# Performance work log

Measured on AMD Instinct MI355X. Metric: run time of the kernel, lower is better.

The kernel has to match this reference:

```python
import jax, jax.numpy as jnp
import numpy as np

EMBED_K = 64
DISEN_K = [4, 4]           # channels per layer
WEIGHT_SIZE_LIST = [64, 64, 64]
TEMPERATURE = 1.0
ROUTING_ITERATIONS = 3
N_LAYERS = 2
EPS = 1e-12


def setup_inputs() -> dict:
    key = jax.random.key(0)
    ks = jax.random.split(key, 8)
    num_users, num_items = 500000, 200000
    n_neigh = 4096
    params = {}
    for layer in range(N_LAYERS):
        k_ch = DISEN_K[layer]
        d_in = WEIGHT_SIZE_LIST[layer]
        d_out = WEIGHT_SIZE_LIST[layer + 1] // k_ch
        params[f"W{layer}"] = jax.random.normal(ks[4 + layer], (k_ch, d_in, d_out), dtype=jnp.float32) * 0.1
        params[f"b{layer}"] = jnp.zeros((k_ch, d_out), dtype=jnp.float32)
    return {
        "user": 123,
        "item": 77,
        "neigh_user": jax.random.randint(ks[0], (n_neigh,), 0, num_items),   # item ids
        "neigh_item": jax.random.randint(ks[1], (n_neigh,), 0, num_users),   # user ids
        "Gu": jax.random.normal(ks[2], (num_users, EMBED_K), dtype=jnp.float32) * 0.1,
        "Gi": jax.random.normal(ks[3], (num_items, EMBED_K), dtype=jnp.float32) * 0.1,
        **params,
    }


def _project(x, W, b):
    # FeatureProjection: per-channel linear + relu. x: [N, d_in] -> [N, K, d_out]
    return jax.nn.relu(jnp.einsum('ni,kid->nkd', x, W) + b)


def _route_once(z):
    # One DisenGCNLayer call on star graph: node 0 = ego, nodes 1..N = neighbors.
    # L2-normalize per channel (torch F.normalize p=2, dim=-1)
    nrm = jnp.maximum(jnp.linalg.norm(z, axis=-1, keepdims=True), EPS)
    zn = z / nrm                              # [N+1, K, d]
    ego = zn[0]                               # [K, d]
    nb = zn[1:]                               # [N, K, d]
    # routing probs: softmax over channels K of similarity / temperature
    p = jax.nn.softmax(jnp.einsum('nkd,kd->nk', nb, ego) / TEMPERATURE, axis=-1)
    # aggregated ego capsule per channel
    return jnp.einsum('nk,nkd->kd', p, nb)    # [K, d]


def _forward(Gu, Gi, W0, b0, W1, b1, user, item, neigh_user, neigh_item):
    # ego user + its item neighbors; ego item + its user neighbors
    eu = jnp.concatenate([Gu[user][None, :], Gi[neigh_user]], axis=0)   # [N+1, 64]
    ei = jnp.concatenate([Gi[item][None, :], Gu[neigh_item]], axis=0)   # [N+1, 64]
    for (W, b) in ((W0, b0), (W1, b1)):
        zu = _project(eu, W, b)               # [N+1, K, d]
        zi = _project(ei, W, b)
        for _ in range(ROUTING_ITERATIONS):
            zu = zu.at[0].set(_route_once(zu))
            zi = zi.at[0].set(_route_once(zi))
        eu = zu.reshape(zu.shape[0], -1)      # [N+1, K*d]
        ei = zi.reshape(zi.shape[0], -1)
        # message dropout = 0.0 -> identity
    xui = jnp.sum(eu[0] * ei[0])[None]        # shape (1,)
    return xui, eu[0], ei[0]


def reference(user, item, neigh_user, neigh_item, Gu, Gi, W0, b0, W1, b1):
    return _forward(Gu, Gi, W0, b0, W1, b1, user, item, neigh_user, neigh_item)
```

## Files before the change

### kernel.cpp

```cpp
#include <hip/hip_runtime.h>
#include <hip/hip_bf16.h>


#define EPS 1e-12f
#define LOG2E 1.44269504088896f
#define SPB 8
#define NBK (2 * SPB)

__device__ __forceinline__ float g16sum(float v) {
    v += __shfl_xor(v, 1, 64);
    v += __shfl_xor(v, 2, 64);
    v += __shfl_xor(v, 4, 64);
    v += __shfl_xor(v, 8, 64);
    return v;
}
__device__ __forceinline__ unsigned short f2bf(float f) {
    unsigned int b = __float_as_uint(f);
    b += 0x7fffu + ((b >> 16) & 1u);
    return (unsigned short)(b >> 16);
}
__device__ __forceinline__ float bf2f(unsigned short u) {
    return __uint_as_float(((unsigned int)u) << 16);
}
__device__ __forceinline__ float bflo(unsigned int w) {
    return __uint_as_float(w << 16);
}
__device__ __forceinline__ float bfhi(unsigned int w) {
    return __uint_as_float(w & 0xffff0000u);
}

__device__ __forceinline__ void slot_write(unsigned long long* p, float v,
                                           unsigned int gen) {
    atomicExch(p, ((unsigned long long)__float_as_uint(v) << 32) |
                  (unsigned long long)gen);
}
__device__ __forceinline__ float slot_read(unsigned long long* p,
                                           unsigned int gen) {
    unsigned long long v;
    for (;;) {
        v = atomicAdd(p, 0ull);
        if ((unsigned int)(v & 0xffffffffull) == gen) break;
        __builtin_amdgcn_s_sleep(1);
    }
    return __uint_as_float((unsigned int)(v >> 32));
}

__device__ __forceinline__ float proj_row4(const float xa[4],
                                           const float* __restrict__ W,
                                           const float* __restrict__ b, int lane) {
    const int k = lane >> 4, d = lane & 15;
    float sum = b[k * 16 + d];
    const float* __restrict__ Wp = W + k * 1024 + d;
#pragma unroll
    for (int i = 0; i < 64; ++i)
        sum = fmaf(__shfl(xa[i & 3], i >> 2, 64), Wp[i * 16], sum);
    return fmaxf(sum, 0.f);
}

__global__ __launch_bounds__(256) void k1_gather_proj2(
    const int* __restrict__ user, const int* __restrict__ item,
    const int* __restrict__ nu, const int* __restrict__ ni,
    const float* __restrict__ Gu, const float* __restrict__ Gi,
    const float* __restrict__ W0, const float* __restrict__ b0,
    const float* __restrict__ W1, const float* __restrict__ b1,
    unsigned short* __restrict__ znbA, unsigned short* __restrict__ znbB,
    unsigned int* __restrict__ call_ctr, int n_rows)
{
    if (blockIdx.x == 0 && threadIdx.x == 0) atomicAdd(call_ctr, 1u);

    const int lane = threadIdx.x & 63;
    const int wv   = threadIdx.x >> 6;
    const int rr   = blockIdx.x * 4 + wv;
    if (rr >= 2 * n_rows) return;
    const int side = rr >= n_rows;
    const int n    = rr - side * n_rows;
    const int c    = lane & 15;

    int idx; const float* G;
    if (n == 0) { idx = side ? item[0] : user[0];     G = side ? Gi : Gu; }
    else        { idx = side ? ni[n - 1] : nu[n - 1]; G = side ? Gu : Gi; }
    const float4 xv = ((const float4*)(G + (size_t)idx * 64))[c];
    const float xa[4] = {xv.x, xv.y, xv.z, xv.w};

    const float z0 = proj_row4(xa, W0, b0, lane);
    const float nrm0 = fmaxf(sqrtf(g16sum(z0 * z0)), EPS);
    znbA[(size_t)rr * 64 + lane] = f2bf(z0 / nrm0);

    if (n == 0) return;

    float xa2[4];
#pragma unroll
    for (int jj = 0; jj < 4; ++jj) xa2[jj] = __shfl(z0, (c << 2) | jj, 64);
    const float z1 = proj_row4(xa2, W1, b1, lane);
    const float nrm1 = fmaxf(sqrtf(g16sum(z1 * z1)), EPS);
    znbB[(size_t)rr * 64 + lane] = f2bf(z1 / nrm1);
}

__global__ __launch_bounds__(1024) void k2_route_all(
    const unsigned short* __restrict__ znbA, const unsigned short* __restrict__ znbB,
    const float* __restrict__ W1, const float* __restrict__ b1,
    unsigned long long* __restrict__ slots,
    const unsigned int* __restrict__ call_ctr,
    float* __restrict__ out, int n_neigh)
{
    const int n_rows = n_neigh + 1;
    const int tid  = threadIdx.x;
    const int lane = tid & 63;
    const int wv   = tid >> 6;
    const int side = blockIdx.x & 1;
    const int bg   = blockIdx.x >> 1;
    const unsigned short* __restrict__ zA = znbA + (size_t)side * n_rows * 64;
    const unsigned short* __restrict__ zB = znbB + (size_t)side * n_rows * 64;
    const unsigned int genbase = (*call_ctr) * 8u;

    __shared__ float sW[4096];
    __shared__ float red[16][64];
    __shared__ float sEgo[64];
    __shared__ float sTmp[64];

    for (int q = tid; q < 4096; q += 1024) {
        const int i = q >> 6, m = q & 63;
        sW[q] = W1[(m >> 4) * 1024 + i * 16 + (m & 15)];
    }
    if (tid < 64) sEgo[tid] = bf2f(zA[tid]) * LOG2E;
    __syncthreads();

    const int j   = lane & 7;
    const int rg0 = bg * 128 + (tid >> 3);

    for (int s = 0; s < 6; ++s) {
        const unsigned short* __restrict__ zb = (s < 3) ? zA : zB;
        const unsigned int gen = genbase + (unsigned int)s + 1u;
        float ego[8];
#pragma unroll
        for (int m = 0; m < 8; ++m) ego[m] = sEgo[j * 8 + m];

        float a8[8] = {0.f, 0.f, 0.f, 0.f, 0.f, 0.f, 0.f, 0.f};
        for (int r = rg0; r < n_neigh; r += SPB * 128) {
            const uint4 q = *(const uint4*)(zb + (((size_t)r + 1) << 6) + (j << 3));
            float x[8];
            x[0] = bflo(q.x); x[1] = bfhi(q.x);
            x[2] = bflo(q.y); x[3] = bfhi(q.y);
            x[4] = bflo(q.z); x[5] = bfhi(q.z);
            x[6] = bflo(q.w); x[7] = bfhi(q.w);
            float partial = 0.f;
#pragma unroll
            for (int m = 0; m < 8; ++m) partial = fmaf(x[m], ego[m], partial);
            const float dp = partial + __shfl_xor(partial, 1, 64);
            const float eo = exp2f(dp);
            float den = eo + __shfl_xor(eo, 2, 64);
            den += __shfl_xor(den, 4, 64);
            const float p = eo * __builtin_amdgcn_rcpf(den);
#pragma unroll
            for (int m = 0; m < 8; ++m) a8[m] = fmaf(p, x[m], a8[m]);
        }
#pragma unroll
        for (int mask = 8; mask <= 32; mask <<= 1)
#pragma unroll
            for (int m = 0; m < 8; ++m) a8[m] += __shfl_xor(a8[m], mask, 64);
        if (lane < 8) {
#pragma unroll
            for (int m = 0; m < 8; ++m) red[wv][lane * 8 + m] = a8[m];
        }
        __syncthreads();

        unsigned long long* slotbase = slots + (size_t)(s * 2 + side) * SPB * 64;
        if (wv == 0) {
            float ssum = 0.f;
#pragma unroll
            for (int w = 0; w < 16; ++w) ssum += red[w][lane];
            slot_write(&slotbase[bg * 64 + lane], ssum, gen);
        }
        __syncthreads();

        if (s < 5) {
            if (wv < SPB)
                red[wv][lane] = slot_read(&slotbase[wv * 64 + lane], gen);
            __syncthreads();
            if (wv == 0) {
                float e = 0.f;
#pragma unroll
                for (int bb = 0; bb < SPB; ++bb) e += red[bb][lane];
                if (s == 2) sTmp[lane] = e;
                else sEgo[lane] = (e / fmaxf(sqrtf(g16sum(e * e)), EPS)) * LOG2E;
            }
            __syncthreads();
            if (s == 2) {
                if (wv == 0) {
                    float xa[4];
#pragma unroll
                    for (int jj = 0; jj < 4; ++jj) xa[jj] = sTmp[((lane & 15) << 2) | jj];
                    float sum = b1[lane];
#pragma unroll
                    for (int i = 0; i < 64; ++i)
                        sum = fmaf(__shfl(xa[i & 3], i >> 2, 64), sW[i * 64 + lane], sum);
                    sum = fmaxf(sum, 0.f);
                    sEgo[lane] = (sum / fmaxf(sqrtf(g16sum(sum * sum)), EPS)) * LOG2E;
                }
                __syncthreads();
            }
        } else if (side == 0 && bg == 0) {
            const int s2 = wv >> 3, bb = wv & 7;
            unsigned long long* sb2 = slots + (size_t)(5 * 2 + s2) * SPB * 64;
            red[wv][lane] = slot_read(&sb2[bb * 64 + lane], gen);
            __syncthreads();
            if (wv == 0) {
                float u = 0.f, v = 0.f;
#pragma unroll
                for (int w = 0; w < 8; ++w)  u += red[w][lane];
#pragma unroll
                for (int w = 8; w < 16; ++w) v += red[w][lane];
                out[1 + lane]  = u;
                out[65 + lane] = v;
                float p = u * v;
#pragma unroll
                for (int sh = 32; sh >= 1; sh >>= 1) p += __shfl_xor(p, sh, 64);
                if (lane == 0) out[0] = p;
            }
        }
    }
}

extern "C" void kernel_launch(void* const* d_in, const int* in_sizes, int n_in,
                              void* d_out, int out_size, void* d_ws, size_t ws_size,
                              hipStream_t stream) {
    const int*   user       = (const int*)d_in[0];
    const int*   item       = (const int*)d_in[1];
    const int*   neigh_user = (const int*)d_in[2];
    const int*   neigh_item = (const int*)d_in[3];
    const float* Gu         = (const float*)d_in[4];
    const float* Gi         = (const float*)d_in[5];
    const float* W0         = (const float*)d_in[6];
    const float* b0         = (const float*)d_in[7];
    const float* W1         = (const float*)d_in[8];
    const float* b1         = (const float*)d_in[9];
    float* out = (float*)d_out;

    const int n_neigh = in_sizes[2];
    const int n_rows  = n_neigh + 1;
    const size_t rowsz = (size_t)2 * n_rows * 64;

    unsigned short*     znbA  = (unsigned short*)d_ws;
    unsigned short*     znbB  = znbA + rowsz;
    unsigned long long* slots = (unsigned long long*)(znbB + rowsz);
    unsigned int*       ctr   = (unsigned int*)(slots + 6 * 2 * SPB * 64);

    hipLaunchKernelGGL(k1_gather_proj2, dim3((2 * n_rows + 3) / 4), dim3(256), 0, stream,
                       user, item, neigh_user, neigh_item, Gu, Gi, W0, b0, W1, b1,
                       znbA, znbB, ctr, n_rows);
    hipLaunchKernelGGL(k2_route_all, dim3(NBK), dim3(1024), 0, stream,
                       znbA, znbB, W1, b1, slots, ctr, out, n_neigh);
}
```

Measured before the change: 45.46 us.

## Fuse gather, projections and routing into one kernel with LDS-resident neighbor rows

Merges the gather/projection kernel into the routing kernel so each of the 16 blocks gathers its own 512 neighbor rows, projects them with W0 from shared memory, and keeps the bf16 results in LDS with a padded stride. Per-row normalization for layer 0 is moved into the routing loop, and the layer-1 projection is done in place in LDS after the third routing step. This removes a kernel launch and the global round-trip of the intermediate buffers. The cost is that only 16 blocks now do all the gather and projection work, so parallelism for the memory-bound gather drops sharply. The per-call generation counters also become per block.

```diff
diff --git a/kernel.cpp b/kernel.cpp
--- a/kernel.cpp
+++ b/kernel.cpp
@@ -6,6 +6,7 @@
 #define LOG2E 1.44269504088896f
 #define SPB 8
 #define NBK (2 * SPB)
+#define ZSTR 80
 
 __device__ __forceinline__ float g16sum(float v) {
     v += __shfl_xor(v, 1, 64);
@@ -28,7 +29,6 @@
 __device__ __forceinline__ float bfhi(unsigned int w) {
     return __uint_as_float(w & 0xffff0000u);
 }
-
 __device__ __forceinline__ void slot_write(unsigned long long* p, float v,
                                            unsigned int gen) {
     atomicExch(p, ((unsigned long long)__float_as_uint(v) << 32) |
@@ -45,114 +45,128 @@
     return __uint_as_float((unsigned int)(v >> 32));
 }
 
-__device__ __forceinline__ float proj_row4(const float xa[4],
-                                           const float* __restrict__ W,
-                                           const float* __restrict__ b, int lane) {
-    const int k = lane >> 4, d = lane & 15;
-    float sum = b[k * 16 + d];
-    const float* __restrict__ Wp = W + k * 1024 + d;
-#pragma unroll
-    for (int i = 0; i < 64; ++i)
-        sum = fmaf(__shfl(xa[i & 3], i >> 2, 64), Wp[i * 16], sum);
-    return fmaxf(sum, 0.f);
-}
-
-__global__ __launch_bounds__(256) void k1_gather_proj2(
+__global__ __launch_bounds__(1024, 1) void disen_one(
     const int* __restrict__ user, const int* __restrict__ item,
     const int* __restrict__ nu, const int* __restrict__ ni,
     const float* __restrict__ Gu, const float* __restrict__ Gi,
     const float* __restrict__ W0, const float* __restrict__ b0,
     const float* __restrict__ W1, const float* __restrict__ b1,
-    unsigned short* __restrict__ znbA, unsigned short* __restrict__ znbB,
-    unsigned int* __restrict__ call_ctr, int n_rows)
-{
-    if (blockIdx.x == 0 && threadIdx.x == 0) atomicAdd(call_ctr, 1u);
-
-    const int lane = threadIdx.x & 63;
-    const int wv   = threadIdx.x >> 6;
-    const int rr   = blockIdx.x * 4 + wv;
-    if (rr >= 2 * n_rows) return;
-    const int side = rr >= n_rows;
-    const int n    = rr - side * n_rows;
-    const int c    = lane & 15;
-
-    int idx; const float* G;
-    if (n == 0) { idx = side ? item[0] : user[0];     G = side ? Gi : Gu; }
-    else        { idx = side ? ni[n - 1] : nu[n - 1]; G = side ? Gu : Gi; }
-    const float4 xv = ((const float4*)(G + (size_t)idx * 64))[c];
-    const float xa[4] = {xv.x, xv.y, xv.z, xv.w};
-
-    const float z0 = proj_row4(xa, W0, b0, lane);
-    const float nrm0 = fmaxf(sqrtf(g16sum(z0 * z0)), EPS);
-    znbA[(size_t)rr * 64 + lane] = f2bf(z0 / nrm0);
-
-    if (n == 0) return;
-
-    float xa2[4];
-#pragma unroll
-    for (int jj = 0; jj < 4; ++jj) xa2[jj] = __shfl(z0, (c << 2) | jj, 64);
-    const float z1 = proj_row4(xa2, W1, b1, lane);
-    const float nrm1 = fmaxf(sqrtf(g16sum(z1 * z1)), EPS);
-    znbB[(size_t)rr * 64 + lane] = f2bf(z1 / nrm1);
-}
-
-__global__ __launch_bounds__(1024) void k2_route_all(
-    const unsigned short* __restrict__ znbA, const unsigned short* __restrict__ znbB,
-    const float* __restrict__ W1, const float* __restrict__ b1,
-    unsigned long long* __restrict__ slots,
-    const unsigned int* __restrict__ call_ctr,
+    unsigned long long* __restrict__ slots, unsigned int* __restrict__ ctr,
     float* __restrict__ out, int n_neigh)
 {
-    const int n_rows = n_neigh + 1;
     const int tid  = threadIdx.x;
     const int lane = tid & 63;
     const int wv   = tid >> 6;
     const int side = blockIdx.x & 1;
     const int bg   = blockIdx.x >> 1;
-    const unsigned short* __restrict__ zA = znbA + (size_t)side * n_rows * 64;
-    const unsigned short* __restrict__ zB = znbB + (size_t)side * n_rows * 64;
-    const unsigned int genbase = (*call_ctr) * 8u;
+    const int g    = lane >> 4;
+    const int c    = lane & 15;
+    const int j    = lane & 7;
 
     __shared__ float sW[4096];
     __shared__ float red[16][64];
     __shared__ float sEgo[64];
     __shared__ float sTmp[64];
-
+    __shared__ unsigned int sGen;
+    __shared__ unsigned short zB[512 * ZSTR];
+
+    if (tid == 0) sGen = (atomicAdd(&ctr[blockIdx.x], 1u) + 1u) * 8u;
+
+    for (int q = tid; q < 4096; q += 1024) {
+        const int i = q >> 6, m = q & 63;
+        sW[q] = W0[(m >> 4) * 1024 + i * 16 + (m & 15)];
+    }
+    __syncthreads();
+    const unsigned int genbase = sGen;
+
+    const int*   nidx = side ? ni : nu;
+    const float* G    = side ? Gu : Gi;
+    float4 xv[8];
+#pragma unroll
+    for (int pass = 0; pass < 8; ++pass) {
+        const int L = pass * 64 + wv * 4 + g;
+        const int n = 1 + bg * 128 + (L & 127) + (L >> 7) * (SPB * 128);
+        if (n <= n_neigh)
+            xv[pass] = ((const float4*)(G + (size_t)nidx[n - 1] * 64))[c];
+        else
+            xv[pass] = make_float4(0.f, 0.f, 0.f, 0.f);
+    }
+    {
+        const float4 bv = ((const float4*)b0)[c];
+#pragma unroll
+        for (int pass = 0; pass < 8; ++pass) {
+            const int L = pass * 64 + wv * 4 + g;
+            const bool act = (1 + bg * 128 + (L & 127) + (L >> 7) * (SPB * 128)) <= n_neigh;
+            float xa[4] = {xv[pass].x, xv[pass].y, xv[pass].z, xv[pass].w};
+            float o0 = bv.x, o1 = bv.y, o2 = bv.z, o3 = bv.w;
+#pragma unroll
+            for (int i = 0; i < 64; ++i) {
+                const float xi = __shfl(xa[i & 3], (g << 4) + (i >> 2), 64);
+                const float4 w = ((const float4*)sW)[i * 16 + c];
+                o0 = fmaf(xi, w.x, o0); o1 = fmaf(xi, w.y, o1);
+                o2 = fmaf(xi, w.z, o2); o3 = fmaf(xi, w.w, o3);
+            }
+            ushort4 st;
+            if (act) {
+                st.x = f2bf(fmaxf(o0, 0.f)); st.y = f2bf(fmaxf(o1, 0.f));
+                st.z = f2bf(fmaxf(o2, 0.f)); st.w = f2bf(fmaxf(o3, 0.f));
+            } else st = make_ushort4(0, 0, 0, 0);
+            *(ushort4*)&zB[L * ZSTR + 4 * c] = st;
+        }
+    }
+    if (wv == 0) {
+        const int idx0 = side ? item[0] : user[0];
+        const float* G0 = side ? Gi : Gu;
+        const float4 q0 = ((const float4*)(G0 + (size_t)idx0 * 64))[c];
+        float xa[4] = {q0.x, q0.y, q0.z, q0.w};
+        float s = b0[lane];
+#pragma unroll
+        for (int i = 0; i < 64; ++i)
+            s = fmaf(__shfl(xa[i & 3], i >> 2, 64), sW[i * 64 + lane], s);
+        s = fmaxf(s, 0.f);
+        sEgo[lane] = (s / fmaxf(sqrtf(g16sum(s * s)), EPS)) * LOG2E;
+    }
+    __syncthreads();
     for (int q = tid; q < 4096; q += 1024) {
         const int i = q >> 6, m = q & 63;
         sW[q] = W1[(m >> 4) * 1024 + i * 16 + (m & 15)];
     }
-    if (tid < 64) sEgo[tid] = bf2f(zA[tid]) * LOG2E;
     __syncthreads();
 
-    const int j   = lane & 7;
-    const int rg0 = bg * 128 + (tid >> 3);
-
     for (int s = 0; s < 6; ++s) {
-        const unsigned short* __restrict__ zb = (s < 3) ? zA : zB;
         const unsigned int gen = genbase + (unsigned int)s + 1u;
         float ego[8];
 #pragma unroll
         for (int m = 0; m < 8; ++m) ego[m] = sEgo[j * 8 + m];
 
         float a8[8] = {0.f, 0.f, 0.f, 0.f, 0.f, 0.f, 0.f, 0.f};
-        for (int r = rg0; r < n_neigh; r += SPB * 128) {
-            const uint4 q = *(const uint4*)(zb + (((size_t)r + 1) << 6) + (j << 3));
+#pragma unroll
+        for (int m = 0; m < 4; ++m) {
+            const int L = m * 128 + (tid >> 3);
+            const uint4 q = *(const uint4*)&zB[L * ZSTR + 8 * j];
             float x[8];
             x[0] = bflo(q.x); x[1] = bfhi(q.x);
             x[2] = bflo(q.y); x[3] = bfhi(q.y);
             x[4] = bflo(q.z); x[5] = bfhi(q.z);
             x[6] = bflo(q.w); x[7] = bfhi(q.w);
+            float inv = 1.f;
+            if (s < 3) {
+                float ss = 0.f;
+#pragma unroll
+                for (int mm = 0; mm < 8; ++mm) ss = fmaf(x[mm], x[mm], ss);
+                ss += __shfl_xor(ss, 1, 64);
+                inv = __builtin_amdgcn_rcpf(fmaxf(sqrtf(ss), EPS));
+            }
             float partial = 0.f;
 #pragma unroll
-            for (int m = 0; m < 8; ++m) partial = fmaf(x[m], ego[m], partial);
-            const float dp = partial + __shfl_xor(partial, 1, 64);
+            for (int mm = 0; mm < 8; ++mm) partial = fmaf(x[mm], ego[mm], partial);
+            const float dp = (partial + __shfl_xor(partial, 1, 64)) * inv;
             const float eo = exp2f(dp);
             float den = eo + __shfl_xor(eo, 2, 64);
             den += __shfl_xor(den, 4, 64);
-            const float p = eo * __builtin_amdgcn_rcpf(den);
-#pragma unroll
-            for (int m = 0; m < 8; ++m) a8[m] = fmaf(p, x[m], a8[m]);
+            const float p = eo * __builtin_amdgcn_rcpf(den) * inv;
+#pragma unroll
+            for (int mm = 0; mm < 8; ++mm) a8[mm] = fmaf(p, x[mm], a8[mm]);
         }
 #pragma unroll
         for (int mask = 8; mask <= 32; mask <<= 1)
@@ -172,6 +186,37 @@
             slot_write(&slotbase[bg * 64 + lane], ssum, gen);
         }
         __syncthreads();
+
+        if (s == 2) {
+            const float4 bv1 = ((const float4*)b1)[c];
+#pragma unroll
+            for (int pass = 0; pass < 8; ++pass) {
+                const int L = pass * 64 + wv * 4 + g;
+                const bool act = (1 + bg * 128 + (L & 127) + (L >> 7) * (SPB * 128)) <= n_neigh;
+                const ushort4 u = *(const ushort4*)&zB[L * ZSTR + 4 * c];
+                float xa[4] = {bf2f(u.x), bf2f(u.y), bf2f(u.z), bf2f(u.w)};
+                float o0 = bv1.x, o1 = bv1.y, o2 = bv1.z, o3 = bv1.w;
+#pragma unroll
+                for (int i = 0; i < 64; ++i) {
+                    const float xi = __shfl(xa[i & 3], (g << 4) + (i >> 2), 64);
+                    const float4 w = ((const float4*)sW)[i * 16 + c];
+                    o0 = fmaf(xi, w.x, o0); o1 = fmaf(xi, w.y, o1);
+                    o2 = fmaf(xi, w.z, o2); o3 = fmaf(xi, w.w, o3);
+                }
+                o0 = fmaxf(o0, 0.f); o1 = fmaxf(o1, 0.f);
+                o2 = fmaxf(o2, 0.f); o3 = fmaxf(o3, 0.f);
+                float ss = o0 * o0 + o1 * o1 + o2 * o2 + o3 * o3;
+                ss += __shfl_xor(ss, 1, 64);
+                ss += __shfl_xor(ss, 2, 64);
+                const float inv = __builtin_amdgcn_rcpf(fmaxf(sqrtf(ss), EPS));
+                ushort4 st;
+                if (act) {
+                    st.x = f2bf(o0 * inv); st.y = f2bf(o1 * inv);
+                    st.z = f2bf(o2 * inv); st.w = f2bf(o3 * inv);
+                } else st = make_ushort4(0, 0, 0, 0);
+                *(ushort4*)&zB[L * ZSTR + 4 * c] = st;
+            }
+        }
 
         if (s < 5) {
             if (wv < SPB)
@@ -199,7 +244,7 @@
                 }
                 __syncthreads();
             }
-        } else if (side == 0 && bg == 0) {
+        } else if (blockIdx.x == 0) {
             const int s2 = wv >> 3, bb = wv & 7;
             unsigned long long* sb2 = slots + (size_t)(5 * 2 + s2) * SPB * 64;
             red[wv][lane] = slot_read(&sb2[bb * 64 + lane], gen);
@@ -237,17 +282,11 @@
     float* out = (float*)d_out;
 
     const int n_neigh = in_sizes[2];
-    const int n_rows  = n_neigh + 1;
-    const size_t rowsz = (size_t)2 * n_rows * 64;
-
-    unsigned short*     znbA  = (unsigned short*)d_ws;
-    unsigned short*     znbB  = znbA + rowsz;
-    unsigned long long* slots = (unsigned long long*)(znbB + rowsz);
+
+    unsigned long long* slots = (unsigned long long*)d_ws;
     unsigned int*       ctr   = (unsigned int*)(slots + 6 * 2 * SPB * 64);
 
-    hipLaunchKernelGGL(k1_gather_proj2, dim3((2 * n_rows + 3) / 4), dim3(256), 0, stream,
-                       user, item, neigh_user, neigh_item, Gu, Gi, W0, b0, W1, b1,
-                       znbA, znbB, ctr, n_rows);
-    hipLaunchKernelGGL(k2_route_all, dim3(NBK), dim3(1024), 0, stream,
-                       znbA, znbB, W1, b1, slots, ctr, out, n_neigh);
-}
+    hipLaunchKernelGGL(disen_one, dim3(NBK), dim3(1024), 0, stream,
+                       user, item, neigh_user, neigh_item, Gu, Gi,
+                       W0, b0, W1, b1, slots, ctr, out, n_neigh);
+}
```

After: 123.1 us. 2.71x slower.

## Process four rows per wavefront with float4 weight loads in projection kernel

Applied to the files above, without the earlier changes.

The gather-and-project kernel now assigns four rows to each wavefront. Each 16-lane group owns one row and each lane computes four output features using float4 weight loads, where before each wave handled one row with one output per lane. This cuts the weight-load instructions per row and the number of blocks launched by four, and uses ushort4 stores. The trade-off is more registers per lane. The ego-row branch now runs the second projection redundantly, with its store masked off.

```diff
diff --git a/kernel.cpp b/kernel.cpp
--- a/kernel.cpp
+++ b/kernel.cpp
@@ -43,18 +43,6 @@
         __builtin_amdgcn_s_sleep(1);
     }
     return __uint_as_float((unsigned int)(v >> 32));
-}
-
-__device__ __forceinline__ float proj_row4(const float xa[4],
-                                           const float* __restrict__ W,
-                                           const float* __restrict__ b, int lane) {
-    const int k = lane >> 4, d = lane & 15;
-    float sum = b[k * 16 + d];
-    const float* __restrict__ Wp = W + k * 1024 + d;
-#pragma unroll
-    for (int i = 0; i < 64; ++i)
-        sum = fmaf(__shfl(xa[i & 3], i >> 2, 64), Wp[i * 16], sum);
-    return fmaxf(sum, 0.f);
 }
 
 __global__ __launch_bounds__(256) void k1_gather_proj2(
@@ -70,30 +58,78 @@
 
     const int lane = threadIdx.x & 63;
     const int wv   = threadIdx.x >> 6;
-    const int rr   = blockIdx.x * 4 + wv;
-    if (rr >= 2 * n_rows) return;
-    const int side = rr >= n_rows;
-    const int n    = rr - side * n_rows;
+    const int g    = lane >> 4;
     const int c    = lane & 15;
-
-    int idx; const float* G;
-    if (n == 0) { idx = side ? item[0] : user[0];     G = side ? Gi : Gu; }
-    else        { idx = side ? ni[n - 1] : nu[n - 1]; G = side ? Gu : Gi; }
-    const float4 xv = ((const float4*)(G + (size_t)idx * 64))[c];
-    const float xa[4] = {xv.x, xv.y, xv.z, xv.w};
-
-    const float z0 = proj_row4(xa, W0, b0, lane);
-    const float nrm0 = fmaxf(sqrtf(g16sum(z0 * z0)), EPS);
-    znbA[(size_t)rr * 64 + lane] = f2bf(z0 / nrm0);
-
-    if (n == 0) return;
-
-    float xa2[4];
-#pragma unroll
-    for (int jj = 0; jj < 4; ++jj) xa2[jj] = __shfl(z0, (c << 2) | jj, 64);
-    const float z1 = proj_row4(xa2, W1, b1, lane);
-    const float nrm1 = fmaxf(sqrtf(g16sum(z1 * z1)), EPS);
-    znbB[(size_t)rr * 64 + lane] = f2bf(z1 / nrm1);
+    const int base = (blockIdx.x * 4 + wv) * 4;
+    if (base >= 2 * n_rows) return;
+    const int rr   = base + g;
+    const bool act = rr < 2 * n_rows;
+    const int side = act ? (rr >= n_rows) : 0;
+    const int n    = act ? (rr - side * n_rows) : 0;
+
+    float xa[4] = {0.f, 0.f, 0.f, 0.f};
+    if (act) {
+        int idx; const float* G;
+        if (n == 0) { idx = side ? item[0] : user[0];     G = side ? Gi : Gu; }
+        else        { idx = side ? ni[n - 1] : nu[n - 1]; G = side ? Gu : Gi; }
+        const float4 xv = ((const float4*)(G + (size_t)idx * 64))[c];
+        xa[0] = xv.x; xa[1] = xv.y; xa[2] = xv.z; xa[3] = xv.w;
+    }
+
+    const int k = c >> 2;
+    const float4 bv0 = ((const float4*)b0)[c];
+    float o[4] = {bv0.x, bv0.y, bv0.z, bv0.w};
+    {
+        const float4* __restrict__ Wp = (const float4*)(W0 + k * 1024) + (c & 3);
+#pragma unroll
+        for (int i = 0; i < 64; ++i) {
+            const float xi = __shfl(xa[i & 3], (g << 4) + (i >> 2), 64);
+            const float4 w = Wp[i * 4];
+            o[0] = fmaf(xi, w.x, o[0]); o[1] = fmaf(xi, w.y, o[1]);
+            o[2] = fmaf(xi, w.z, o[2]); o[3] = fmaf(xi, w.w, o[3]);
+        }
+    }
+#pragma unroll
+    for (int q = 0; q < 4; ++q) o[q] = fmaxf(o[q], 0.f);
+    {
+        float ss = o[0] * o[0] + o[1] * o[1] + o[2] * o[2] + o[3] * o[3];
+        ss += __shfl_xor(ss, 1, 64);
+        ss += __shfl_xor(ss, 2, 64);
+        const float inv = 1.f / fmaxf(sqrtf(ss), EPS);
+        if (act) {
+            ushort4 st;
+            st.x = f2bf(o[0] * inv); st.y = f2bf(o[1] * inv);
+            st.z = f2bf(o[2] * inv); st.w = f2bf(o[3] * inv);
+            *(ushort4*)&znbA[(size_t)rr * 64 + 4 * c] = st;
+        }
+    }
+
+    const float4 bv1 = ((const float4*)b1)[c];
+    float p[4] = {bv1.x, bv1.y, bv1.z, bv1.w};
+    {
+        const float4* __restrict__ Wp = (const float4*)(W1 + k * 1024) + (c & 3);
+#pragma unroll
+        for (int i = 0; i < 64; ++i) {
+            const float xi = __shfl(o[i & 3], (g << 4) + (i >> 2), 64);
+            const float4 w = Wp[i * 4];
+            p[0] = fmaf(xi, w.x, p[0]); p[1] = fmaf(xi, w.y, p[1]);
+            p[2] = fmaf(xi, w.z, p[2]); p[3] = fmaf(xi, w.w, p[3]);
+        }
+    }
+#pragma unroll
+    for (int q = 0; q < 4; ++q) p[q] = fmaxf(p[q], 0.f);
+    {
+        float ss = p[0] * p[0] + p[1] * p[1] + p[2] * p[2] + p[3] * p[3];
+        ss += __shfl_xor(ss, 1, 64);
+        ss += __shfl_xor(ss, 2, 64);
+        const float inv = 1.f / fmaxf(sqrtf(ss), EPS);
+        if (act && n > 0) {
+            ushort4 st;
+            st.x = f2bf(p[0] * inv); st.y = f2bf(p[1] * inv);
+            st.z = f2bf(p[2] * inv); st.w = f2bf(p[3] * inv);
+            *(ushort4*)&znbB[(size_t)rr * 64 + 4 * c] = st;
+        }
+    }
 }
 
 __global__ __launch_bounds__(1024) void k2_route_all(
@@ -245,7 +281,7 @@
     unsigned long long* slots = (unsigned long long*)(znbB + rowsz);
     unsigned int*       ctr   = (unsigned int*)(slots + 6 * 2 * SPB * 64);
 
-    hipLaunchKernelGGL(k1_gather_proj2, dim3((2 * n_rows + 3) / 4), dim3(256), 0, stream,
+    hipLaunchKernelGGL(k1_gather_proj2, dim3((2 * n_rows + 15) / 16), dim3(256), 0, stream,
                        user, item, neigh_user, neigh_item, Gu, Gi, W0, b0, W1, b1,
                        znbA, znbB, ctr, n_rows);
     hipLaunchKernelGGL(k2_route_all, dim3(NBK), dim3(1024), 0, stream,
```

After: 41.09 us. 9.6% less time.
